# Optimization experiments

Hardware: AMD Instinct MI355X
Metric: run time of the kernel (lower is better)

Reference implementation:

```python
import jax, jax.numpy as jnp
import numpy as np

D = 4          # bundle dim
NB = 16        # num_bundles
TOTAL = D * NB # 64
MAX_DEGREE = 10
T_DIFF = 1.0


def _sage_conv(x, edge_index, Wl, Wr, b):
    # PyG SAGEConv (mean aggr): out = lin_l(mean_{j->i} x_j) + lin_r(x_i)
    n = x.shape[0]
    src, dst = edge_index[0], edge_index[1]
    msum = jax.ops.segment_sum(x[src], dst, num_segments=n)
    cnt = jax.ops.segment_sum(jnp.ones((src.shape[0],), x.dtype), dst, num_segments=n)
    mean = msum / jnp.maximum(cnt, 1.0)[:, None]
    return mean @ Wl.T + x @ Wr.T + b


def _cayley(params):
    # params: [n, d(d-1)/2] -> skew A (row-major upper triangle) -> O = (I-A)^{-1}(I+A)
    n = params.shape[0]
    iu, ju = np.triu_indices(D, 1)
    A = jnp.zeros((n, D, D), params.dtype)
    A = A.at[:, iu, ju].set(params).at[:, ju, iu].set(-params)
    I = jnp.eye(D, dtype=params.dtype)
    return jnp.linalg.solve(I[None] - A, jnp.broadcast_to(I, (n, D, D)) + A)


def _heat_kernel(edge_index, n, t):
    # H(t) = exp(-t L_sym) via Taylor; L = I - D^-1/2 A D^-1/2 with self-loops
    loops = jnp.stack([jnp.arange(n), jnp.arange(n)])
    ei = jnp.concatenate([edge_index, loops], axis=1)
    row, col = ei[0], ei[1]
    deg = jax.ops.segment_sum(jnp.ones(row.shape, jnp.float32), row, num_segments=n)
    dis = jnp.where(deg > 0, deg ** -0.5, 0.0)
    adj = jnp.zeros((n, n), jnp.float32).at[row, col].set(1.0)
    L = jnp.eye(n, dtype=jnp.float32) - dis[:, None] * adj * dis[None, :]
    result = jnp.eye(n, dtype=jnp.float32)
    term = jnp.eye(n, dtype=jnp.float32)
    for k in range(1, MAX_DEGREE + 1):
        term = (-t / k) * (L @ term)
        result = result + term
    return result


def reference(x, edge_index, Wl1, Wr1, b1, Wl2, Wr2, b2, Wp, bp, W, bias):
    n = x.shape[0]
    h = jax.nn.relu(_sage_conv(x, edge_index, Wl1, Wr1, b1))
    h = jax.nn.relu(_sage_conv(h, edge_index, Wl2, Wr2, b2))
    params = h @ Wp.T + bp
    O = _cayley(params)
    # block-diagonal O applied per bundle: rotate to bundle frame (O^T x)
    xb = x.reshape(n, NB, D)
    local = jnp.einsum('nji,nbj->nbi', O, xb).reshape(n, TOTAL)
    # heat diffusion
    H = _heat_kernel(edge_index, n, T_DIFF)
    diffused = H @ local
    # channel mixing + rotate back + bias + activation
    mixed = (diffused @ W).reshape(n, NB, D)
    back = jnp.einsum('nij,nbj->nbi', O, mixed).reshape(n, TOTAL)
    return jax.nn.relu(back + bias)


def setup_inputs() -> dict:
    key = jax.random.key(0)
    ks = jax.random.split(key, 12)
    n, E = 4096, 131072
    x = jax.random.normal(ks[0], (n, TOTAL), jnp.float32)
    edge_index = jax.random.randint(ks[1], (2, E), 0, n)
    Wl1 = jax.random.normal(ks[2], (32, 64), jnp.float32) * 0.1
    Wr1 = jax.random.normal(ks[3], (32, 64), jnp.float32) * 0.1
    b1 = jnp.zeros((32,), jnp.float32)
    Wl2 = jax.random.normal(ks[4], (16, 32), jnp.float32) * 0.1
    Wr2 = jax.random.normal(ks[5], (16, 32), jnp.float32) * 0.1
    b2 = jnp.zeros((16,), jnp.float32)
    Wp = jax.random.normal(ks[6], (D * (D - 1) // 2, 16), jnp.float32) * 0.1
    bp = jnp.zeros((D * (D - 1) // 2,), jnp.float32)
    Wq, _ = jnp.linalg.qr(jax.random.normal(ks[7], (TOTAL, TOTAL), jnp.float32))
    bias = jnp.zeros((TOTAL,), jnp.float32)
    return {"x": x, "edge_index": edge_index, "Wl1": Wl1, "Wr1": Wr1, "b1": b1,
            "Wl2": Wl2, "Wr2": Wr2, "b2": b2, "Wp": Wp, "bp": bp, "W": Wq, "bias": bias}
```

## Files before the change

kernel.cpp:

```cpp
#include <hip/hip_runtime.h>
#include <stdint.h>
#include <stddef.h>


#define CAP 96

#define CHEB_C0 0.4657596f
#define CHEB_C1 0.4158209f
#define CHEB_C2 0.0998776f
#define CHEB_C3 0.0163106f

__global__ void zero_kernel(int* __restrict__ pos, int* __restrict__ opos, int n) {
    int t = blockIdx.x * blockDim.x + threadIdx.x;
    if (t < n) { pos[t] = 0; opos[t] = 0; }
}

__global__ void edge_kernel(const int* __restrict__ ei, int E,
                            int* __restrict__ pos, int* __restrict__ opos,
                            int* __restrict__ in_cols, int* __restrict__ out_cols) {
    int t = blockIdx.x * blockDim.x + threadIdx.x;
    int base = t << 2;
    if (base >= E) return;
    if (base + 4 <= E) {
        int4 s4 = *(const int4*)(ei + base);
        int4 d4 = *(const int4*)(ei + E + base);
        int s, d, sl;
        s = s4.x; d = d4.x;
        sl = atomicAdd(&pos[d], 1);  if (sl < CAP) in_cols[(size_t)d * CAP + sl] = s;
        sl = atomicAdd(&opos[s], 1); if (sl < CAP) out_cols[(size_t)s * CAP + sl] = d;
        s = s4.y; d = d4.y;
        sl = atomicAdd(&pos[d], 1);  if (sl < CAP) in_cols[(size_t)d * CAP + sl] = s;
        sl = atomicAdd(&opos[s], 1); if (sl < CAP) out_cols[(size_t)s * CAP + sl] = d;
        s = s4.z; d = d4.z;
        sl = atomicAdd(&pos[d], 1);  if (sl < CAP) in_cols[(size_t)d * CAP + sl] = s;
        sl = atomicAdd(&opos[s], 1); if (sl < CAP) out_cols[(size_t)s * CAP + sl] = d;
        s = s4.w; d = d4.w;
        sl = atomicAdd(&pos[d], 1);  if (sl < CAP) in_cols[(size_t)d * CAP + sl] = s;
        sl = atomicAdd(&opos[s], 1); if (sl < CAP) out_cols[(size_t)s * CAP + sl] = d;
    } else {
        for (int e = base; e < E; ++e) {
            int s = ei[e], d = ei[E + e];
            int sl = atomicAdd(&pos[d], 1);
            if (sl < CAP) in_cols[(size_t)d * CAP + sl] = s;
            sl = atomicAdd(&opos[s], 1);
            if (sl < CAP) out_cols[(size_t)s * CAP + sl] = d;
        }
    }
}

__global__ void rowg1s1_kernel(const int* __restrict__ out_cols,
                               const int* __restrict__ opos, const int* __restrict__ pos,
                               const int* __restrict__ in_cols,
                               const float* __restrict__ x,
                               const float* __restrict__ Wl1, const float* __restrict__ Wr1,
                               const float* __restrict__ b1,
                               int* __restrict__ ncol, float* __restrict__ nwgt,
                               int* __restrict__ rowcnt,
                               float* __restrict__ h1, int n) {
    int row = blockIdx.x * (blockDim.x >> 6) + (threadIdx.x >> 6);
    if (row >= n) return;
    int lane = threadIdx.x & 63;
    int wIB = threadIdx.x >> 6;
    __shared__ unsigned sbm[4][128];
    __shared__ float sA[4][64];
    __shared__ float sB[4][64];

    {
        sbm[wIB][lane] = 0u;
        sbm[wIB][64 + lane] = 0u;
        int odeg = opos[row];
        int oe = (odeg > CAP) ? CAP : odeg;
        const int* ob = out_cols + (size_t)row * CAP;
        for (int i = lane; i < oe; i += 64) {
            int d = ob[i];
            atomicOr(&sbm[wIB][d >> 5], 1u << (d & 31));
        }
        if (lane == 0) atomicOr(&sbm[wIB][row >> 5], 1u << (row & 31));
        __syncthreads();
        unsigned w0 = sbm[wIB][lane * 2];
        unsigned w1 = sbm[wIB][lane * 2 + 1];
        int c = __popc(w0) + __popc(w1);
        int incl = c;
        for (int d = 1; d < 64; d <<= 1) {
            int v = __shfl_up(incl, d, 64);
            if (lane >= d) incl += v;
        }
        int idx = incl - c;
        float disr = rsqrtf((float)odeg + 1.0f);
        int* oc = ncol + (size_t)row * CAP;
        float* ow = nwgt + (size_t)row * CAP;
        for (int k = 0; k < 2; ++k) {
            unsigned word = k ? w1 : w0;
            int wbase = (lane * 2 + k) << 5;
            while (word) {
                int b = __ffs(word) - 1;
                word &= word - 1;
                int j = wbase + b;
                if (idx < CAP) {
                    oc[idx] = j;
                    ow[idx] = disr * rsqrtf((float)opos[j] + 1.0f);
                }
                ++idx;
            }
        }
        int cnt = __shfl(incl, 63, 64);
        if (cnt > CAP) cnt = CAP;
        int padded = (cnt + 15) & ~15;
        if (padded > CAP) padded = CAP;
        if (lane < padded - cnt) {
            oc[cnt + lane] = 0;
            ow[cnt + lane] = 0.0f;
        }
        if (lane == 0) rowcnt[row] = padded;
    }

    const int* base = in_cols + (size_t)row * CAP;
    int cnt = pos[row];
    float rc = 1.0f / fmaxf((float)cnt, 1.0f);
    int e = (cnt > CAP) ? CAP : cnt;
    float acc = 0.f;
    int i = 0;
    for (; i + 16 <= e; i += 16) {
        int4 c0 = *(const int4*)(base + i);
        int4 c1 = *(const int4*)(base + i + 4);
        int4 c2 = *(const int4*)(base + i + 8);
        int4 c3 = *(const int4*)(base + i + 12);
        float t0 = x[((size_t)c0.x << 6) + lane], t1 = x[((size_t)c0.y << 6) + lane];
        float t2 = x[((size_t)c0.z << 6) + lane], t3 = x[((size_t)c0.w << 6) + lane];
        float t4 = x[((size_t)c1.x << 6) + lane], t5 = x[((size_t)c1.y << 6) + lane];
        float t6 = x[((size_t)c1.z << 6) + lane], t7 = x[((size_t)c1.w << 6) + lane];
        float t8 = x[((size_t)c2.x << 6) + lane], t9 = x[((size_t)c2.y << 6) + lane];
        float ta = x[((size_t)c2.z << 6) + lane], tb = x[((size_t)c2.w << 6) + lane];
        float tc = x[((size_t)c3.x << 6) + lane], td = x[((size_t)c3.y << 6) + lane];
        float te = x[((size_t)c3.z << 6) + lane], tf = x[((size_t)c3.w << 6) + lane];
        acc += (((t0 + t1) + (t2 + t3)) + ((t4 + t5) + (t6 + t7)))
             + (((t8 + t9) + (ta + tb)) + ((tc + td) + (te + tf)));
    }
    for (; i + 8 <= e; i += 8) {
        int4 ca = *(const int4*)(base + i);
        int4 cb = *(const int4*)(base + i + 4);
        float t0 = x[((size_t)ca.x << 6) + lane], t1 = x[((size_t)ca.y << 6) + lane];
        float t2 = x[((size_t)ca.z << 6) + lane], t3 = x[((size_t)ca.w << 6) + lane];
        float t4 = x[((size_t)cb.x << 6) + lane], t5 = x[((size_t)cb.y << 6) + lane];
        float t6 = x[((size_t)cb.z << 6) + lane], t7 = x[((size_t)cb.w << 6) + lane];
        acc += ((t0 + t1) + (t2 + t3)) + ((t4 + t5) + (t6 + t7));
    }
    for (; i < e; ++i) acc += x[((size_t)base[i] << 6) + lane];
    sA[wIB][lane] = acc;
    sB[wIB][lane] = x[((size_t)row << 6) + lane];
    int o = lane & 31;
    const float* wrow = (lane < 32) ? (Wl1 + o * 64) : (Wr1 + o * 64);
    const float* vrow = (lane < 32) ? sA[wIB] : sB[wIB];
    float d = 0.f;
#pragma unroll 8
    for (int f = 0; f < 64; ++f) d += vrow[f] * wrow[f];
    float other = __shfl_xor(d, 32, 64);
    if (lane < 32)
        h1[(size_t)row * 32 + o] = fmaxf(b1[o] + d * rc + other, 0.f);
}

__global__ void g2cr_kernel(const int* __restrict__ in_cols, const int* __restrict__ pos,
                            const float* __restrict__ x, const float* __restrict__ h1,
                            const float* __restrict__ Wl2, const float* __restrict__ Wr2,
                            const float* __restrict__ b2,
                            const float* __restrict__ Wp, const float* __restrict__ bp,
                            float* __restrict__ Og, float* __restrict__ termA,
                            float* __restrict__ out, int n) {
    int row = blockIdx.x * (blockDim.x >> 6) + (threadIdx.x >> 6);
    if (row >= n) return;
    int lane = threadIdx.x & 63;
    int wIB = threadIdx.x >> 6;
    __shared__ float sA[4][64];
    __shared__ float sB[4][64];
    const int* base = in_cols + (size_t)row * CAP;
    int cnt = pos[row];
    float rc = 1.0f / fmaxf((float)cnt, 1.0f);
    int e = (cnt > CAP) ? CAP : cnt;
    int f = lane & 31, half = lane >> 5;
    float a0 = 0.f, a1 = 0.f, a2 = 0.f, a3 = 0.f;
    int i = 0;
    for (; i + 8 <= e; i += 8) {
        int c0 = base[i + half];
        int c1 = base[i + 2 + half];
        int c2 = base[i + 4 + half];
        int c3 = base[i + 6 + half];
        a0 += h1[((size_t)c0 << 5) + f];
        a1 += h1[((size_t)c1 << 5) + f];
        a2 += h1[((size_t)c2 << 5) + f];
        a3 += h1[((size_t)c3 << 5) + f];
    }
    for (; i + half < e; i += 2) a0 += h1[((size_t)base[i + half] << 5) + f];
    float acc = (a0 + a1) + (a2 + a3);
    acc += __shfl_xor(acc, 32, 64);
    if (lane < 32) {
        sA[wIB][lane] = acc;
        sB[wIB][lane] = h1[(size_t)row * 32 + lane];
    }
    int o16 = lane & 15, hi = (lane >> 4) & 1;
    float dsum = 0.f;
    if (lane < 32) {
        const float* vrow = hi ? sB[wIB] : sA[wIB];
        const float* wmat = hi ? Wr2 : Wl2;
#pragma unroll 8
        for (int f2 = 0; f2 < 32; ++f2) dsum += vrow[f2] * wmat[o16 * 32 + f2];
    }
    float oth = __shfl_xor(dsum, 16, 64);
    if (lane < 16)
        sA[wIB][32 + o16] = fmaxf(b2[o16] + dsum * rc + oth, 0.f);
    if (lane == 0) {
        float pp[6];
#pragma unroll
        for (int oo = 0; oo < 6; ++oo) {
            float a = bp[oo];
#pragma unroll
            for (int ff = 0; ff < 16; ++ff) a += sA[wIB][32 + ff] * Wp[oo * 16 + ff];
            pp[oo] = a;
        }
        float A[4][4] = {{0.f,    pp[0],  pp[1],  pp[2]},
                         {-pp[0], 0.f,    pp[3],  pp[4]},
                         {-pp[1], -pp[3], 0.f,    pp[5]},
                         {-pp[2], -pp[4], -pp[5], 0.f}};
        float M[4][4], R[4][4];
#pragma unroll
        for (int r = 0; r < 4; ++r)
#pragma unroll
            for (int c = 0; c < 4; ++c) {
                float id = (r == c) ? 1.f : 0.f;
                M[r][c] = id - A[r][c];
                R[r][c] = id + A[r][c];
            }
#pragma unroll
        for (int k = 0; k < 4; ++k) {
            float inv = 1.0f / M[k][k];
#pragma unroll
            for (int c = 0; c < 4; ++c) { M[k][c] *= inv; R[k][c] *= inv; }
#pragma unroll
            for (int r = 0; r < 4; ++r) {
                if (r == k) continue;
                float fk = M[r][k];
#pragma unroll
                for (int c = 0; c < 4; ++c) { M[r][c] -= fk * M[k][c]; R[r][c] -= fk * R[k][c]; }
            }
        }
#pragma unroll
        for (int r = 0; r < 4; ++r)
#pragma unroll
            for (int c = 0; c < 4; ++c) sB[wIB][32 + r * 4 + c] = R[r][c];
    }
    if (lane < 16) {
        Og[(size_t)row * 16 + lane] = sB[wIB][32 + lane];
        float4 xv = *(const float4*)(x + (size_t)row * 64 + lane * 4);
        float4 r;
        r.x = sB[wIB][32+0]*xv.x + sB[wIB][32+4]*xv.y + sB[wIB][32+8]*xv.z  + sB[wIB][32+12]*xv.w;
        r.y = sB[wIB][32+1]*xv.x + sB[wIB][32+5]*xv.y + sB[wIB][32+9]*xv.z  + sB[wIB][32+13]*xv.w;
        r.z = sB[wIB][32+2]*xv.x + sB[wIB][32+6]*xv.y + sB[wIB][32+10]*xv.z + sB[wIB][32+14]*xv.w;
        r.w = sB[wIB][32+3]*xv.x + sB[wIB][32+7]*xv.y + sB[wIB][32+11]*xv.z + sB[wIB][32+15]*xv.w;
        *(float4*)(termA + (size_t)row * 64 + lane * 4) = r;
        float4 s = make_float4(CHEB_C0 * r.x, CHEB_C0 * r.y, CHEB_C0 * r.z, CHEB_C0 * r.w);
        *(float4*)(out + (size_t)row * 64 + lane * 4) = s;
    }
}

template <int MODE>
__global__ void cheb_kernel(const int* __restrict__ rowcnt,
                            const int* __restrict__ ncol, const float* __restrict__ nwgt,
                            const float* __restrict__ gbuf, float* __restrict__ obuf,
                            float* __restrict__ out, float c, int n,
                            const float* __restrict__ Og,
                            const float* __restrict__ W,
                            const float* __restrict__ bias) {
    int row = blockIdx.x * (blockDim.x >> 6) + (threadIdx.x >> 6);
    if (row >= n) return;
    int lane = threadIdx.x & 63;
    const int* cbase = ncol + (size_t)row * CAP;
    const float* wbase = nwgt + (size_t)row * CAP;
    int e = rowcnt[row];
    float acc = 0.f;
    for (int i = 0; i < e; i += 16) {
        int4 c0 = *(const int4*)(cbase + i);
        int4 c1 = *(const int4*)(cbase + i + 4);
        int4 c2 = *(const int4*)(cbase + i + 8);
        int4 c3 = *(const int4*)(cbase + i + 12);
        float4 w0 = *(const float4*)(wbase + i);
        float4 w1 = *(const float4*)(wbase + i + 4);
        float4 w2 = *(const float4*)(wbase + i + 8);
        float4 w3 = *(const float4*)(wbase + i + 12);
        float t0 = gbuf[((size_t)c0.x << 6) + lane], t1 = gbuf[((size_t)c0.y << 6) + lane];
        float t2 = gbuf[((size_t)c0.z << 6) + lane], t3 = gbuf[((size_t)c0.w << 6) + lane];
        float t4 = gbuf[((size_t)c1.x << 6) + lane], t5 = gbuf[((size_t)c1.y << 6) + lane];
        float t6 = gbuf[((size_t)c1.z << 6) + lane], t7 = gbuf[((size_t)c1.w << 6) + lane];
        float t8 = gbuf[((size_t)c2.x << 6) + lane], t9 = gbuf[((size_t)c2.y << 6) + lane];
        float ta = gbuf[((size_t)c2.z << 6) + lane], tb = gbuf[((size_t)c2.w << 6) + lane];
        float tc = gbuf[((size_t)c3.x << 6) + lane], td = gbuf[((size_t)c3.y << 6) + lane];
        float te = gbuf[((size_t)c3.z << 6) + lane], tf = gbuf[((size_t)c3.w << 6) + lane];
        acc = fmaf(w0.x, t0, acc); acc = fmaf(w0.y, t1, acc);
        acc = fmaf(w0.z, t2, acc); acc = fmaf(w0.w, t3, acc);
        acc = fmaf(w1.x, t4, acc); acc = fmaf(w1.y, t5, acc);
        acc = fmaf(w1.z, t6, acc); acc = fmaf(w1.w, t7, acc);
        acc = fmaf(w2.x, t8, acc); acc = fmaf(w2.y, t9, acc);
        acc = fmaf(w2.z, ta, acc); acc = fmaf(w2.w, tb, acc);
        acc = fmaf(w3.x, tc, acc); acc = fmaf(w3.y, td, acc);
        acc = fmaf(w3.z, te, acc); acc = fmaf(w3.w, tf, acc);
    }
    size_t idx = ((size_t)row << 6) + lane;
    float sv = acc;
    if (MODE == 0) {
        float val = sv;
        obuf[idx] = val;
        out[idx] += c * val;
    } else if (MODE == 1) {
        float val = 2.0f * sv - obuf[idx];
        obuf[idx] = val;
        out[idx] += c * val;
    } else {
        float val = 2.0f * sv - obuf[idx];
        float d = out[idx] + c * val;
        float mv = 0.f;
#pragma unroll 8
        for (int k = 0; k < 64; ++k)
            mv += __shfl(d, k, 64) * W[k * 64 + lane];
        int b4 = lane & ~3;
        int ii = lane & 3;
        const float* orow = Og + (size_t)row * 16 + ii * 4;
        float back = orow[0] * __shfl(mv, b4 + 0, 64)
                   + orow[1] * __shfl(mv, b4 + 1, 64)
                   + orow[2] * __shfl(mv, b4 + 2, 64)
                   + orow[3] * __shfl(mv, b4 + 3, 64);
        out[idx] = fmaxf(back + bias[lane], 0.f);
    }
}

extern "C" void kernel_launch(void* const* d_in, const int* in_sizes, int n_in,
                              void* d_out, int out_size, void* d_ws, size_t ws_size,
                              hipStream_t stream) {
    const float* x    = (const float*)d_in[0];
    const int*   ei   = (const int*)d_in[1];
    const float* Wl1  = (const float*)d_in[2];
    const float* Wr1  = (const float*)d_in[3];
    const float* b1   = (const float*)d_in[4];
    const float* Wl2  = (const float*)d_in[5];
    const float* Wr2  = (const float*)d_in[6];
    const float* b2   = (const float*)d_in[7];
    const float* Wp   = (const float*)d_in[8];
    const float* bp   = (const float*)d_in[9];
    const float* W    = (const float*)d_in[10];
    const float* bias = (const float*)d_in[11];
    float* out = (float*)d_out;

    int n = in_sizes[0] / 64;
    int E = in_sizes[1] / 2;

    char* ws = (char*)d_ws;
    size_t off = 0;
    int* pos  = (int*)(ws + off); off += (size_t)n * 4;
    int* opos = (int*)(ws + off); off += (size_t)n * 4;
    int* in_cols  = (int*)(ws + off); off += (size_t)n * CAP * 4;
    int* out_cols = (int*)(ws + off); off += (size_t)n * CAP * 4;
    int* ncol     = (int*)(ws + off); off += (size_t)n * CAP * 4;
    float* nwgt   = (float*)(ws + off); off += (size_t)n * CAP * 4;
    int* rowcnt   = (int*)(ws + off); off += (size_t)n * 4;
    float* h1     = (float*)(ws + off); off += (size_t)n * 32 * 4;
    float* Og     = (float*)(ws + off); off += (size_t)n * 16 * 4;
    float* termA  = (float*)(ws + off); off += (size_t)n * 64 * 4;
    float* termB  = (float*)(ws + off); off += (size_t)n * 64 * 4;

    const int tb = 256;
    const int rowsPerBlk = tb / 64;
    const int rowGrid = (n + rowsPerBlk - 1) / rowsPerBlk;

    zero_kernel<<<(n + tb - 1) / tb, tb, 0, stream>>>(pos, opos, n);
    edge_kernel<<<((E >> 2) + tb - 1) / tb, tb, 0, stream>>>(ei, E, pos, opos, in_cols, out_cols);
    rowg1s1_kernel<<<rowGrid, tb, 0, stream>>>(out_cols, opos, pos, in_cols, x, Wl1, Wr1, b1,
                                               ncol, nwgt, rowcnt, h1, n);
    g2cr_kernel<<<rowGrid, tb, 0, stream>>>(in_cols, pos, x, h1, Wl2, Wr2, b2, Wp, bp,
                                            Og, termA, out, n);

    cheb_kernel<0><<<rowGrid, tb, 0, stream>>>(rowcnt, ncol, nwgt, termA, termB, out,
                                               CHEB_C1, n, nullptr, nullptr, nullptr);
    cheb_kernel<1><<<rowGrid, tb, 0, stream>>>(rowcnt, ncol, nwgt, termB, termA, out,
                                               CHEB_C2, n, nullptr, nullptr, nullptr);
    cheb_kernel<2><<<rowGrid, tb, 0, stream>>>(rowcnt, ncol, nwgt, termA, termB, out,
                                               CHEB_C3, n, Og, W, bias);
}
```

Before: 70.86 us.

## Build normalized adjacency in place with duplicate-zeroing and defer Chebyshev accumulation

The neighbor list is no longer deduplicated through a bitmap prefix-scan compaction into a separate ncol array. out_cols is reused in place, the self-loop is appended, and duplicate entries get weight zero via the atomicOr return value. The Chebyshev sum is no longer accumulated into out after every step. Each term goes to its own buffer and the weighted sum is formed once in the final kernel, which removes read-modify-write traffic on out and one workspace array. CAP drops from 96 to 80 to shrink the per-row lists, which risks truncating high-degree rows and may leave duplicates that inflate the padded length.

After: 68.85 us. -2.8%, faster.

```diff
diff --git a/kernel.cpp b/kernel.cpp
--- a/kernel.cpp
+++ b/kernel.cpp
@@ -3,7 +3,7 @@
 #include <stddef.h>
 
 
-#define CAP 96
+#define CAP 80
 
 #define CHEB_C0 0.4657596f
 #define CHEB_C1 0.4158209f
@@ -48,14 +48,13 @@
     }
 }
 
-__global__ void rowg1s1_kernel(const int* __restrict__ out_cols,
+__global__ void rowg1s1_kernel(int* __restrict__ out_cols,
                                const int* __restrict__ opos, const int* __restrict__ pos,
                                const int* __restrict__ in_cols,
                                const float* __restrict__ x,
                                const float* __restrict__ Wl1, const float* __restrict__ Wr1,
                                const float* __restrict__ b1,
-                               int* __restrict__ ncol, float* __restrict__ nwgt,
-                               int* __restrict__ rowcnt,
+                               float* __restrict__ nwgt, int* __restrict__ rowcnt,
                                float* __restrict__ h1, int n) {
     int row = blockIdx.x * (blockDim.x >> 6) + (threadIdx.x >> 6);
     if (row >= n) return;
@@ -69,48 +68,22 @@
         sbm[wIB][lane] = 0u;
         sbm[wIB][64 + lane] = 0u;
         int odeg = opos[row];
-        int oe = (odeg > CAP) ? CAP : odeg;
-        const int* ob = out_cols + (size_t)row * CAP;
-        for (int i = lane; i < oe; i += 64) {
-            int d = ob[i];
-            atomicOr(&sbm[wIB][d >> 5], 1u << (d & 31));
+        int oe = (odeg > CAP - 1) ? (CAP - 1) : odeg;
+        int* oc = out_cols + (size_t)row * CAP;
+        float* ow = nwgt + (size_t)row * CAP;
+        float disr = rsqrtf((float)odeg + 1.0f);
+        for (int i = lane; i <= oe; i += 64) {
+            int d = (i == oe) ? row : oc[i];
+            unsigned bit = 1u << (d & 31);
+            unsigned old = atomicOr(&sbm[wIB][d >> 5], bit);
+            float w = (old & bit) ? 0.0f : disr * rsqrtf((float)opos[d] + 1.0f);
+            if (i == oe) oc[i] = row;
+            ow[i] = w;
         }
-        if (lane == 0) atomicOr(&sbm[wIB][row >> 5], 1u << (row & 31));
-        __syncthreads();
-        unsigned w0 = sbm[wIB][lane * 2];
-        unsigned w1 = sbm[wIB][lane * 2 + 1];
-        int c = __popc(w0) + __popc(w1);
-        int incl = c;
-        for (int d = 1; d < 64; d <<= 1) {
-            int v = __shfl_up(incl, d, 64);
-            if (lane >= d) incl += v;
-        }
-        int idx = incl - c;
-        float disr = rsqrtf((float)odeg + 1.0f);
-        int* oc = ncol + (size_t)row * CAP;
-        float* ow = nwgt + (size_t)row * CAP;
-        for (int k = 0; k < 2; ++k) {
-            unsigned word = k ? w1 : w0;
-            int wbase = (lane * 2 + k) << 5;
-            while (word) {
-                int b = __ffs(word) - 1;
-                word &= word - 1;
-                int j = wbase + b;
-                if (idx < CAP) {
-                    oc[idx] = j;
-                    ow[idx] = disr * rsqrtf((float)opos[j] + 1.0f);
-                }
-                ++idx;
-            }
-        }
-        int cnt = __shfl(incl, 63, 64);
-        if (cnt > CAP) cnt = CAP;
+        int cnt = oe + 1;
         int padded = (cnt + 15) & ~15;
         if (padded > CAP) padded = CAP;
-        if (lane < padded - cnt) {
-            oc[cnt + lane] = 0;
-            ow[cnt + lane] = 0.0f;
-        }
+        for (int i = cnt + lane; i < padded; i += 64) { oc[i] = 0; ow[i] = 0.0f; }
         if (lane == 0) rowcnt[row] = padded;
     }
 
@@ -164,8 +137,7 @@
                             const float* __restrict__ Wl2, const float* __restrict__ Wr2,
                             const float* __restrict__ b2,
                             const float* __restrict__ Wp, const float* __restrict__ bp,
-                            float* __restrict__ Og, float* __restrict__ termA,
-                            float* __restrict__ out, int n) {
+                            float* __restrict__ Og, float* __restrict__ termA, int n) {
     int row = blockIdx.x * (blockDim.x >> 6) + (threadIdx.x >> 6);
     if (row >= n) return;
     int lane = threadIdx.x & 63;
@@ -256,16 +228,15 @@
         r.z = sB[wIB][32+2]*xv.x + sB[wIB][32+6]*xv.y + sB[wIB][32+10]*xv.z + sB[wIB][32+14]*xv.w;
         r.w = sB[wIB][32+3]*xv.x + sB[wIB][32+7]*xv.y + sB[wIB][32+11]*xv.z + sB[wIB][32+15]*xv.w;
         *(float4*)(termA + (size_t)row * 64 + lane * 4) = r;
-        float4 s = make_float4(CHEB_C0 * r.x, CHEB_C0 * r.y, CHEB_C0 * r.z, CHEB_C0 * r.w);
-        *(float4*)(out + (size_t)row * 64 + lane * 4) = s;
     }
 }
 
 template <int MODE>
 __global__ void cheb_kernel(const int* __restrict__ rowcnt,
                             const int* __restrict__ ncol, const float* __restrict__ nwgt,
-                            const float* __restrict__ gbuf, float* __restrict__ obuf,
-                            float* __restrict__ out, float c, int n,
+                            const float* __restrict__ gbuf, const float* __restrict__ prev,
+                            const float* __restrict__ t0buf,
+                            float* __restrict__ tout, int n,
                             const float* __restrict__ Og,
                             const float* __restrict__ W,
                             const float* __restrict__ bias) {
@@ -303,18 +274,16 @@
         acc = fmaf(w3.z, te, acc); acc = fmaf(w3.w, tf, acc);
     }
     size_t idx = ((size_t)row << 6) + lane;
-    float sv = acc;
     if (MODE == 0) {
-        float val = sv;
-        obuf[idx] = val;
-        out[idx] += c * val;
+        tout[idx] = acc;
     } else if (MODE == 1) {
-        float val = 2.0f * sv - obuf[idx];
-        obuf[idx] = val;
-        out[idx] += c * val;
+        tout[idx] = 2.0f * acc - prev[idx];
     } else {
-        float val = 2.0f * sv - obuf[idx];
-        float d = out[idx] + c * val;
+        float t1v = prev[idx];
+        float t3v = 2.0f * acc - t1v;
+        float d = fmaf(CHEB_C0, t0buf[idx],
+                  fmaf(CHEB_C1, t1v,
+                  fmaf(CHEB_C2, gbuf[idx], CHEB_C3 * t3v)));
         float mv = 0.f;
 #pragma unroll 8
         for (int k = 0; k < 64; ++k)
@@ -326,7 +295,7 @@
                    + orow[1] * __shfl(mv, b4 + 1, 64)
                    + orow[2] * __shfl(mv, b4 + 2, 64)
                    + orow[3] * __shfl(mv, b4 + 3, 64);
-        out[idx] = fmaxf(back + bias[lane], 0.f);
+        tout[idx] = fmaxf(back + bias[lane], 0.f);
     }
 }
 
@@ -356,13 +325,13 @@
     int* opos = (int*)(ws + off); off += (size_t)n * 4;
     int* in_cols  = (int*)(ws + off); off += (size_t)n * CAP * 4;
     int* out_cols = (int*)(ws + off); off += (size_t)n * CAP * 4;
-    int* ncol     = (int*)(ws + off); off += (size_t)n * CAP * 4;
     float* nwgt   = (float*)(ws + off); off += (size_t)n * CAP * 4;
     int* rowcnt   = (int*)(ws + off); off += (size_t)n * 4;
     float* h1     = (float*)(ws + off); off += (size_t)n * 32 * 4;
     float* Og     = (float*)(ws + off); off += (size_t)n * 16 * 4;
     float* termA  = (float*)(ws + off); off += (size_t)n * 64 * 4;
     float* termB  = (float*)(ws + off); off += (size_t)n * 64 * 4;
+    float* termC  = (float*)(ws + off); off += (size_t)n * 64 * 4;
 
     const int tb = 256;
     const int rowsPerBlk = tb / 64;
@@ -371,14 +340,14 @@
     zero_kernel<<<(n + tb - 1) / tb, tb, 0, stream>>>(pos, opos, n);
     edge_kernel<<<((E >> 2) + tb - 1) / tb, tb, 0, stream>>>(ei, E, pos, opos, in_cols, out_cols);
     rowg1s1_kernel<<<rowGrid, tb, 0, stream>>>(out_cols, opos, pos, in_cols, x, Wl1, Wr1, b1,
-                                               ncol, nwgt, rowcnt, h1, n);
+                                               nwgt, rowcnt, h1, n);
     g2cr_kernel<<<rowGrid, tb, 0, stream>>>(in_cols, pos, x, h1, Wl2, Wr2, b2, Wp, bp,
-                                            Og, termA, out, n);
-
-    cheb_kernel<0><<<rowGrid, tb, 0, stream>>>(rowcnt, ncol, nwgt, termA, termB, out,
-                                               CHEB_C1, n, nullptr, nullptr, nullptr);
-    cheb_kernel<1><<<rowGrid, tb, 0, stream>>>(rowcnt, ncol, nwgt, termB, termA, out,
-                                               CHEB_C2, n, nullptr, nullptr, nullptr);
-    cheb_kernel<2><<<rowGrid, tb, 0, stream>>>(rowcnt, ncol, nwgt, termA, termB, out,
-                                               CHEB_C3, n, Og, W, bias);
-}
+                                            Og, termA, n);
+
+    cheb_kernel<0><<<rowGrid, tb, 0, stream>>>(rowcnt, out_cols, nwgt, termA, nullptr, nullptr,
+                                               termB, n, nullptr, nullptr, nullptr);
+    cheb_kernel<1><<<rowGrid, tb, 0, stream>>>(rowcnt, out_cols, nwgt, termB, termA, nullptr,
+                                               termC, n, nullptr, nullptr, nullptr);
+    cheb_kernel<2><<<rowGrid, tb, 0, stream>>>(rowcnt, out_cols, nwgt, termC, termB, termA,
+                                               out, n, Og, W, bias);
+}
```
